# Kernel tuning notes

Measured on AMD Instinct MI355X. Metric: run time of the kernel, lower is better.

The kernel has to match this reference:

```python
import jax, jax.numpy as jnp
import numpy as np

V = 32000      # vocab_size
D = 768        # embed_dim / d_model
NL = 2         # attn_layers
BATCH = 2
T = 1024       # seq_len
ED = 2 * D     # d_inner (expand_factor=2)
NS = 16        # d_state
K = 4          # d_conv
DT_RANK = (D + 15) // 16  # ceil(d_model/16) = 48


def setup_inputs():
    key = jax.random.key(0)
    ks = jax.random.split(key, 12)
    nrm = lambda k, shp, s=0.02: (jax.random.normal(k, shp, jnp.float32) * s)
    tokens = jax.random.randint(ks[0], (BATCH, T), 0, V)
    embed = nrm(ks[1], (V, D))
    in_proj_w = nrm(ks[2], (NL, 2 * ED, D))
    conv_w = nrm(ks[3], (NL, ED, 1, K), 0.1)   # depthwise conv kernel (O=ED, I/g=1, K)
    conv_b = jnp.zeros((NL, ED), jnp.float32)
    x_proj_w = nrm(ks[4], (NL, DT_RANK + 2 * NS, ED))
    dt_proj_w = nrm(ks[5], (NL, ED, DT_RANK), 0.05)
    dt_proj_b = nrm(ks[6], (NL, ED), 0.05)
    # S4D real init: A = -[1..NS] per channel
    A_log = jnp.log(jnp.broadcast_to(jnp.arange(1, NS + 1, dtype=jnp.float32), (NL, ED, NS)))
    D_param = jnp.ones((NL, ED), jnp.float32)
    out_proj_w = nrm(ks[7], (NL, D, ED))
    ln_w = jnp.ones((NL, D), jnp.float32)
    ln_b = jnp.zeros((NL, D), jnp.float32)
    head_w = nrm(ks[8], (V, D))
    head_b = jnp.zeros((V,), jnp.float32)
    return {"tokens": tokens, "embed": embed, "in_proj_w": in_proj_w,
            "conv_w": conv_w, "conv_b": conv_b, "x_proj_w": x_proj_w,
            "dt_proj_w": dt_proj_w, "dt_proj_b": dt_proj_b, "A_log": A_log,
            "D_param": D_param, "out_proj_w": out_proj_w, "ln_w": ln_w,
            "ln_b": ln_b, "head_w": head_w, "head_b": head_b}


def silu(x):
    return x * jax.nn.sigmoid(x)


def layer_norm(x, w, b, eps=1e-5):
    mu = jnp.mean(x, axis=-1, keepdims=True)
    var = jnp.mean(jnp.square(x - mu), axis=-1, keepdims=True)
    return (x - mu) * jax.lax.rsqrt(var + eps) * w + b


def mamba_block(x, in_w, cw, cb, xp_w, dt_w, dt_b, a_log, d_par, out_w):
    # x: (B, T, D)
    xz = jnp.einsum('btd,ed->bte', x, in_w)           # (B, T, 2*ED)
    xin, z = jnp.split(xz, 2, axis=-1)                 # each (B, T, ED)
    # causal depthwise conv over time
    xc = jnp.transpose(xin, (0, 2, 1))                 # (B, ED, T)
    xc = jax.lax.conv_general_dilated(
        xc, cw, window_strides=(1,), padding=[(K - 1, 0)],
        dimension_numbers=('NCH', 'OIH', 'NCH'), feature_group_count=ED)
    xc = xc + cb[None, :, None]
    xin = silu(jnp.transpose(xc, (0, 2, 1)))           # (B, T, ED)
    # selective SSM
    A = -jnp.exp(a_log)                                # (ED, NS)
    dbc = jnp.einsum('bte,fe->btf', xin, xp_w)         # (B, T, dt_rank + 2*NS)
    delta = dbc[..., :DT_RANK]
    Bm = dbc[..., DT_RANK:DT_RANK + NS]                # (B, T, NS)
    Cm = dbc[..., DT_RANK + NS:]                       # (B, T, NS)
    delta = jax.nn.softplus(jnp.einsum('btr,er->bte', delta, dt_w) + dt_b)  # (B, T, ED)
    dA = jnp.exp(delta[..., None] * A)                 # (B, T, ED, NS)
    dBx = (delta * xin)[..., None] * Bm[:, :, None, :] # (B, T, ED, NS)

    def step(h, inp):
        dA_t, dBx_t, C_t = inp                         # (B,ED,NS),(B,ED,NS),(B,NS)
        h = dA_t * h + dBx_t
        y = jnp.einsum('ben,bn->be', h, C_t)
        return h, y

    h0 = jnp.zeros((x.shape[0], ED, NS), xin.dtype)
    _, ys = jax.lax.scan(step, h0,
                         (jnp.swapaxes(dA, 0, 1), jnp.swapaxes(dBx, 0, 1),
                          jnp.swapaxes(Cm, 0, 1)))
    y = jnp.swapaxes(ys, 0, 1) + d_par * xin           # (B, T, ED)
    return jnp.einsum('bte,de->btd', y * silu(z), out_w)


def reference(tokens, embed, in_proj_w, conv_w, conv_b, x_proj_w, dt_proj_w,
              dt_proj_b, A_log, D_param, out_proj_w, ln_w, ln_b, head_w, head_b):
    x = embed[tokens]                                  # (B, T, D)
    for l in range(NL):  # note: NO residual, matches x = ln(layer(x))
        x = layer_norm(
            mamba_block(x, in_proj_w[l], conv_w[l], conv_b[l], x_proj_w[l],
                        dt_proj_w[l], dt_proj_b[l], A_log[l], D_param[l],
                        out_proj_w[l]),
            ln_w[l], ln_b[l])
    return jnp.einsum('btd,vd->btv', x, head_w) + head_b
```

## Files before the change

### kernel.cpp

```cpp
#include <hip/hip_runtime.h>
#include <hip/hip_bf16.h>
#include <cstdint>
#include <cstddef>

using u16 = unsigned short;

#define DEV static __device__ __forceinline__

DEV float bf2f(u16 u) {
  unsigned int x = ((unsigned int)u) << 16;
  float f;
  __builtin_memcpy(&f, &x, 4);
  return f;
}

DEV u16 f2bf(float f) {
  unsigned int x;
  __builtin_memcpy(&x, &f, 4);
  unsigned int r = (x + 0x7fffu + ((x >> 16) & 1u)) >> 16;
  return (u16)r;
}

typedef __bf16 bf16x8 __attribute__((ext_vector_type(8)));
typedef float f32x4 __attribute__((ext_vector_type(4)));

DEV f32x4 mfma_bf16(bf16x8 a, bf16x8 b, f32x4 c) {
  return __builtin_amdgcn_mfma_f32_16x16x32_bf16(a, b, c, 0, 0, 0);
}

DEV void async_ld16(const void* g, void* lds) {
  __builtin_amdgcn_global_load_lds((const __attribute__((address_space(1))) void*)g,
                                   (__attribute__((address_space(3))) void*)lds,
                                   16, 0, 0);
}

__global__ __launch_bounds__(256) void k_cvt(const float* __restrict__ src,
                                             u16* __restrict__ dst, int n) {
  for (int i = blockIdx.x * 256 + threadIdx.x; i < n; i += gridDim.x * 256)
    dst[i] = f2bf(src[i]);
}

template <bool SPLIT, bool BIAS>
__global__ __launch_bounds__(256, 2) void gemm_bt(
    const u16* __restrict__ Ahi, const u16* __restrict__ Alo,
    const u16* __restrict__ Bw, float* __restrict__ Cf,
    const float* __restrict__ bias, int M, int N, int K, int ldc) {
  __shared__ __align__(16) u16 sA[128 * 64];
  __shared__ __align__(16) u16 sB[128 * 64];
  __shared__ __align__(16) u16 sAl[SPLIT ? 128 * 64 : 8];

  const int tid = threadIdx.x;
  const int wave = tid >> 6;
  const int lane = tid & 63;
  const int mBase = blockIdx.y * 128;
  const int nBase = blockIdx.x * 128;
  const int wm = wave >> 1;
  const int wn = wave & 1;

  f32x4 acc[4][4];
#pragma unroll
  for (int i = 0; i < 4; ++i)
#pragma unroll
    for (int j = 0; j < 4; ++j) acc[i][j] = f32x4{0.f, 0.f, 0.f, 0.f};

  const int rsub = lane >> 3;
  const int ksub = (lane & 7) * 8;

  for (int k0 = 0; k0 < K; k0 += 64) {
#pragma unroll
    for (int it = 0; it < 4; ++it) {
      const int chunk = it * 4 + wave;
      const int row = chunk * 8 + rsub;
      async_ld16(Ahi + (size_t)(mBase + row) * K + (k0 + ksub), (char*)sA + chunk * 1024);
      if constexpr (SPLIT)
        async_ld16(Alo + (size_t)(mBase + row) * K + (k0 + ksub), (char*)sAl + chunk * 1024);
      int rn = nBase + row;
      if (rn > N - 1) rn = N - 1;
      async_ld16(Bw + (size_t)rn * K + (k0 + ksub), (char*)sB + chunk * 1024);
    }
    __syncthreads();

    const int rr = lane & 15;
    const int q8 = (lane >> 4) * 8;
#pragma unroll
    for (int ks = 0; ks < 64; ks += 32) {
      bf16x8 aH[4], bF[4], aL[4];
#pragma unroll
      for (int i = 0; i < 4; ++i) {
        aH[i] = *(const bf16x8*)(sA + (wm * 64 + i * 16 + rr) * 64 + ks + q8);
        bF[i] = *(const bf16x8*)(sB + (wn * 64 + i * 16 + rr) * 64 + ks + q8);
        if constexpr (SPLIT)
          aL[i] = *(const bf16x8*)(sAl + (wm * 64 + i * 16 + rr) * 64 + ks + q8);
      }
#pragma unroll
      for (int i = 0; i < 4; ++i)
#pragma unroll
        for (int j = 0; j < 4; ++j) {
          acc[i][j] = mfma_bf16(aH[i], bF[j], acc[i][j]);
          if constexpr (SPLIT) acc[i][j] = mfma_bf16(aL[i], bF[j], acc[i][j]);
        }
    }
    __syncthreads();
  }

  const int r0 = (lane >> 4) * 4;
  const int cn = lane & 15;
#pragma unroll
  for (int i = 0; i < 4; ++i) {
    const int mm = mBase + wm * 64 + i * 16 + r0;
#pragma unroll
    for (int j = 0; j < 4; ++j) {
      const int nn = nBase + wn * 64 + j * 16 + cn;
      if (nn < N) {
        float bv = 0.f;
        if constexpr (BIAS) bv = bias[nn];
#pragma unroll
        for (int r = 0; r < 4; ++r)
          Cf[(size_t)(mm + r) * ldc + nn] = acc[i][j][r] + bv;
      }
    }
  }
}

__global__ __launch_bounds__(256) void k_embed(const int* __restrict__ tok,
                                               const float* __restrict__ emb,
                                               u16* __restrict__ xh,
                                               u16* __restrict__ xl) {
  const int m = blockIdx.x;
  const float* src = emb + (size_t)tok[m] * 768;
  for (int d = threadIdx.x; d < 768; d += 256) {
    const float v = src[d];
    const u16 h = f2bf(v);
    xh[(size_t)m * 768 + d] = h;
    xl[(size_t)m * 768 + d] = f2bf(v - bf2f(h));
  }
}

__global__ __launch_bounds__(256) void k_conv(const float* __restrict__ xz,
                                              const float* __restrict__ cw,
                                              const float* __restrict__ cb,
                                              float* __restrict__ xinc,
                                              u16* __restrict__ xih,
                                              u16* __restrict__ xil) {
  const int idx = blockIdx.x * 256 + threadIdx.x;
  const int e = idx % 1536;
  const int m = idx / 1536;
  const int t = m & 1023;
  const int b = m >> 10;
  float acc = cb[e];
#pragma unroll
  for (int k = 0; k < 4; ++k) {
    const int tt = t - 3 + k;
    if (tt >= 0) acc += xz[(size_t)((b << 10) + tt) * 3072 + e] * cw[e * 4 + k];
  }
  const float s = acc / (1.f + __expf(-acc));
  xinc[idx] = s;
  const u16 h = f2bf(s);
  xih[idx] = h;
  xil[idx] = f2bf(s - bf2f(h));
}

__global__ __launch_bounds__(256) void k_dt(const float* __restrict__ dbc,
                                            const float* __restrict__ dtw,
                                            const float* __restrict__ dtb,
                                            float* __restrict__ delta) {
  const int m = blockIdx.x;
  __shared__ float sd[48];
  if (threadIdx.x < 48) sd[threadIdx.x] = dbc[m * 80 + threadIdx.x];
  __syncthreads();
  for (int e = threadIdx.x; e < 1536; e += 256) {
    float acc = dtb[e];
#pragma unroll
    for (int r = 0; r < 48; ++r) acc += sd[r] * dtw[e * 48 + r];
    const float sp = (acc > 20.f) ? acc : log1pf(__expf(acc));
    delta[m * 1536 + e] = sp;
  }
}

#define SCAN_NC 16
#define SCAN_CL 64

__global__ __launch_bounds__(256) void k_scan1(
    const float* __restrict__ delta, const float* __restrict__ xinc,
    const float* __restrict__ dbc, const float* __restrict__ alog,
    float* __restrict__ chP, float* __restrict__ chQ) {
  const int b = blockIdx.y;
  const int c = blockIdx.z;
  const int e = blockIdx.x * 16 + (threadIdx.x >> 4);
  const int n = threadIdx.x & 15;
  const float Aen = -__expf(alog[e * 16 + n]);
  const int m0 = (b << 10) + c * SCAN_CL;
  float h = 0.f, P = 1.f;
  float dl = delta[m0 * 1536 + e];
  float xi = xinc[m0 * 1536 + e];
  float Bn = dbc[m0 * 80 + 48 + n];
  for (int t = 0; t < SCAN_CL; ++t) {
    const float dl_c = dl, xi_c = xi, Bn_c = Bn;
    if (t < SCAN_CL - 1) {
      const int m2 = m0 + t + 1;
      dl = delta[m2 * 1536 + e];
      xi = xinc[m2 * 1536 + e];
      Bn = dbc[m2 * 80 + 48 + n];
    }
    const float dA = __expf(dl_c * Aen);
    P *= dA;
    h = dA * h + (dl_c * xi_c) * Bn_c;
  }
  const size_t idx = (((size_t)b * SCAN_NC + c) * 1536 + e) * 16 + n;
  chP[idx] = P;
  chQ[idx] = h;
}

__global__ __launch_bounds__(256) void k_scan_fix(const float* __restrict__ chP,
                                                  const float* __restrict__ chQ,
                                                  float* __restrict__ hst) {
  const int b = blockIdx.y;
  const int e = blockIdx.x * 16 + (threadIdx.x >> 4);
  const int n = threadIdx.x & 15;
  float h = 0.f;
#pragma unroll
  for (int c = 0; c < SCAN_NC; ++c) {
    const size_t idx = (((size_t)b * SCAN_NC + c) * 1536 + e) * 16 + n;
    hst[idx] = h;
    h = chP[idx] * h + chQ[idx];
  }
}

__global__ __launch_bounds__(256) void k_scan2(
    const float* __restrict__ delta, const float* __restrict__ xinc,
    const float* __restrict__ dbc, const float* __restrict__ xz,
    const float* __restrict__ alog, const float* __restrict__ dpar,
    const float* __restrict__ hst, u16* __restrict__ ymh,
    u16* __restrict__ yml) {
  const int b = blockIdx.y;
  const int c = blockIdx.z;
  const int e = blockIdx.x * 16 + (threadIdx.x >> 4);
  const int n = threadIdx.x & 15;
  const float Aen = -__expf(alog[e * 16 + n]);
  const float dp = dpar[e];
  const int m0 = (b << 10) + c * SCAN_CL;
  float h = hst[(((size_t)b * SCAN_NC + c) * 1536 + e) * 16 + n];
  float dl = delta[m0 * 1536 + e];
  float xi = xinc[m0 * 1536 + e];
  float Bn = dbc[m0 * 80 + 48 + n];
  float Cn = dbc[m0 * 80 + 64 + n];
  float zz = xz[(size_t)m0 * 3072 + 1536 + e];
  for (int t = 0; t < SCAN_CL; ++t) {
    const float dl_c = dl, xi_c = xi, Bn_c = Bn, Cn_c = Cn, zz_c = zz;
    if (t < SCAN_CL - 1) {
      const int m2 = m0 + t + 1;
      dl = delta[m2 * 1536 + e];
      xi = xinc[m2 * 1536 + e];
      Bn = dbc[m2 * 80 + 48 + n];
      Cn = dbc[m2 * 80 + 64 + n];
      zz = xz[(size_t)m2 * 3072 + 1536 + e];
    }
    const float dA = __expf(dl_c * Aen);
    h = dA * h + (dl_c * xi_c) * Bn_c;
    float p = h * Cn_c;
    p += __shfl_xor(p, 1);
    p += __shfl_xor(p, 2);
    p += __shfl_xor(p, 4);
    p += __shfl_xor(p, 8);
    if (n == 0) {
      const float y = p + dp * xi_c;
      const float sz = zz_c / (1.f + __expf(-zz_c));
      const float ym = y * sz;
      const int mt = m0 + t;
      const u16 hh = f2bf(ym);
      ymh[mt * 1536 + e] = hh;
      yml[mt * 1536 + e] = f2bf(ym - bf2f(hh));
    }
  }
}

__global__ __launch_bounds__(256) void k_ln(const float* __restrict__ g,
                                            const float* __restrict__ w,
                                            const float* __restrict__ bb,
                                            u16* __restrict__ xh,
                                            u16* __restrict__ xl) {
  const int m = blockIdx.x;
  const float* row = g + (size_t)m * 768;
  const int tid = threadIdx.x;
  const float v0 = row[tid], v1 = row[tid + 256], v2 = row[tid + 512];
  float s = v0 + v1 + v2;
#pragma unroll
  for (int o = 32; o > 0; o >>= 1) s += __shfl_xor(s, o);
  __shared__ float red[4];
  if ((tid & 63) == 0) red[tid >> 6] = s;
  __syncthreads();
  const float mu = (red[0] + red[1] + red[2] + red[3]) * (1.f / 768.f);
  const float d0 = v0 - mu, d1 = v1 - mu, d2 = v2 - mu;
  float q = d0 * d0 + d1 * d1 + d2 * d2;
#pragma unroll
  for (int o = 32; o > 0; o >>= 1) q += __shfl_xor(q, o);
  __syncthreads();
  if ((tid & 63) == 0) red[tid >> 6] = q;
  __syncthreads();
  const float var = (red[0] + red[1] + red[2] + red[3]) * (1.f / 768.f);
  const float rs = rsqrtf(var + 1e-5f);
  const float dd[3] = {d0, d1, d2};
#pragma unroll
  for (int i = 0; i < 3; ++i) {
    const int d = tid + i * 256;
    const float y = dd[i] * rs * w[d] + bb[d];
    const u16 h = f2bf(y);
    xh[(size_t)m * 768 + d] = h;
    xl[(size_t)m * 768 + d] = f2bf(y - bf2f(h));
  }
}

extern "C" void kernel_launch(void* const* d_in, const int* in_sizes, int n_in,
                              void* d_out, int out_size, void* d_ws, size_t ws_size,
                              hipStream_t stream) {
  const int* tokens = (const int*)d_in[0];
  const float* embed = (const float*)d_in[1];
  const float* in_w = (const float*)d_in[2];
  const float* conv_w = (const float*)d_in[3];
  const float* conv_b = (const float*)d_in[4];
  const float* xp_w = (const float*)d_in[5];
  const float* dt_w = (const float*)d_in[6];
  const float* dt_b = (const float*)d_in[7];
  const float* A_log = (const float*)d_in[8];
  const float* D_par = (const float*)d_in[9];
  const float* out_w = (const float*)d_in[10];
  const float* ln_w = (const float*)d_in[11];
  const float* ln_b = (const float*)d_in[12];
  const float* head_w = (const float*)d_in[13];
  const float* head_b = (const float*)d_in[14];

  char* p = (char*)d_ws;
  auto alloc = [&](size_t bytes) {
    char* r = p;
    p += (bytes + 255) & ~(size_t)255;
    return r;
  };
  float* xz = (float*)alloc(2048ull * 3072 * 4);
  float* xinc = (float*)alloc(2048ull * 1536 * 4);
  u16* xih = (u16*)alloc(2048ull * 1536 * 2);
  u16* xil = (u16*)alloc(2048ull * 1536 * 2);
  float* dbc = (float*)alloc(2048ull * 80 * 4);
  float* delta = (float*)alloc(2048ull * 1536 * 4);
  u16* ymh = (u16*)alloc(2048ull * 1536 * 2);
  u16* yml = (u16*)alloc(2048ull * 1536 * 2);
  float* gout = (float*)alloc(2048ull * 768 * 4);
  u16* xh = (u16*)alloc(2048ull * 768 * 2);
  u16* xl = (u16*)alloc(2048ull * 768 * 2);
  u16* w_in_h = (u16*)alloc(2ull * 3072 * 768 * 2);
  u16* w_xp_h = (u16*)alloc(2ull * 80 * 1536 * 2);
  u16* w_out_h = (u16*)alloc(2ull * 768 * 1536 * 2);
  u16* w_head_h = (u16*)alloc(32000ull * 768 * 2);
  float* chP = (float*)alloc(2ull * SCAN_NC * 1536 * 16 * 4);
  float* chQ = (float*)alloc(2ull * SCAN_NC * 1536 * 16 * 4);
  float* hst = (float*)alloc(2ull * SCAN_NC * 1536 * 16 * 4);

  k_cvt<<<2048, 256, 0, stream>>>(in_w, w_in_h, 2 * 3072 * 768);
  k_cvt<<<256, 256, 0, stream>>>(xp_w, w_xp_h, 2 * 80 * 1536);
  k_cvt<<<1024, 256, 0, stream>>>(out_w, w_out_h, 2 * 768 * 1536);
  k_cvt<<<4096, 256, 0, stream>>>(head_w, w_head_h, 32000 * 768);

  k_embed<<<2048, 256, 0, stream>>>(tokens, embed, xh, xl);

  for (int l = 0; l < 2; ++l) {
    gemm_bt<true, false><<<dim3(24, 16), 256, 0, stream>>>(
        xh, xl, w_in_h + (size_t)l * 2359296, xz, nullptr, 2048, 3072, 768, 3072);

    k_conv<<<12288, 256, 0, stream>>>(xz, conv_w + l * 6144, conv_b + l * 1536, xinc, xih, xil);

    gemm_bt<true, false><<<dim3(1, 16), 256, 0, stream>>>(
        xih, xil, w_xp_h + (size_t)l * 122880, dbc, nullptr, 2048, 80, 1536, 80);

    k_dt<<<2048, 256, 0, stream>>>(dbc, dt_w + (size_t)l * 73728, dt_b + l * 1536, delta);

    k_scan1<<<dim3(96, 2, SCAN_NC), 256, 0, stream>>>(
        delta, xinc, dbc, A_log + l * 24576, chP, chQ);
    k_scan_fix<<<dim3(96, 2), 256, 0, stream>>>(chP, chQ, hst);
    k_scan2<<<dim3(96, 2, SCAN_NC), 256, 0, stream>>>(
        delta, xinc, dbc, xz, A_log + l * 24576, D_par + l * 1536, hst, ymh, yml);

    gemm_bt<true, false><<<dim3(6, 16), 256, 0, stream>>>(
        ymh, yml, w_out_h + (size_t)l * 1179648, gout, nullptr, 2048, 768, 1536, 768);

    k_ln<<<2048, 256, 0, stream>>>(gout, ln_w + l * 768, ln_b + l * 768, xh, xl);
  }

  gemm_bt<true, true><<<dim3(250, 16), 256, 0, stream>>>(
      xh, xl, w_head_h, (float*)d_out, head_b, 2048, 32000, 768, 32000);
}
```

Before: 1.316 ms.

## Add double-buffered 128x256 swizzled GEMM and split-K atomics for skinny GEMMs

Adds a new 512-thread GEMM kernel with 128x256 tiles, double-buffered async LDS staging, XOR-swizzled LDS layout, workgroup remapping and MFMA priority hints. It is used for the in_proj and head projections. The x_proj and out_proj GEMMs switch to split-K with atomicAdd into zero-initialised outputs to expose more parallelism. The cost is extra zeroing kernels and atomic traffic, and float atomics make the accumulation order non-deterministic.

```diff
diff --git a/kernel.cpp b/kernel.cpp
--- a/kernel.cpp
+++ b/kernel.cpp
@@ -40,11 +40,130 @@
     dst[i] = f2bf(src[i]);
 }
 
+__global__ __launch_bounds__(256) void k_zero(float* __restrict__ p, int n) {
+  const int i = blockIdx.x * 256 + threadIdx.x;
+  if (i < n) p[i] = 0.f;
+}
+
 template <bool SPLIT, bool BIAS>
+__global__ __launch_bounds__(512, 2) void gemm2(
+    const u16* __restrict__ Ahi, const u16* __restrict__ Alo,
+    const u16* __restrict__ Bw, float* __restrict__ Cf,
+    const float* __restrict__ bias, int M, int N, int K, int ldc) {
+  __shared__ __align__(16) u16 sA[2][128 * 64];
+  __shared__ __align__(16) u16 sAl[SPLIT ? 2 : 1][128 * 64];
+  __shared__ __align__(16) u16 sB[2][256 * 64];
+
+  const int tid = threadIdx.x;
+  const int wave = tid >> 6;
+  const int lane = tid & 63;
+  const int nwg = gridDim.x;
+  const int w = (blockIdx.x & 7) * (nwg >> 3) + (blockIdx.x >> 3);
+  const int mBlocks = M >> 7;
+  const int mb = w % mBlocks;
+  const int nb = w / mBlocks;
+  const int mBase = mb * 128;
+  const int nBase = nb * 256;
+  const int wm = wave >> 2;
+  const int wn = wave & 3;
+
+  f32x4 acc[4][4];
+#pragma unroll
+  for (int i = 0; i < 4; ++i)
+#pragma unroll
+    for (int j = 0; j < 4; ++j) acc[i][j] = f32x4{0.f, 0.f, 0.f, 0.f};
+
+  const int rl = lane >> 3;
+  const int sw = (lane & 7) ^ rl;
+
+  auto stage = [&](int bf, int k0) {
+    const int koff = k0 + sw * 8;
+#pragma unroll
+    for (int r = 0; r < 2; ++r) {
+      const int row = r * 64 + wave * 8;
+      async_ld16(Ahi + (size_t)(mBase + row + rl) * K + koff,
+                 (u16*)sA[bf] + row * 64);
+    }
+    if constexpr (SPLIT) {
+#pragma unroll
+      for (int r = 0; r < 2; ++r) {
+        const int row = r * 64 + wave * 8;
+        async_ld16(Alo + (size_t)(mBase + row + rl) * K + koff,
+                   (u16*)sAl[bf] + row * 64);
+      }
+    }
+#pragma unroll
+    for (int r = 0; r < 4; ++r) {
+      const int row = r * 64 + wave * 8;
+      async_ld16(Bw + (size_t)(nBase + row + rl) * K + koff,
+                 (u16*)sB[bf] + row * 64);
+    }
+  };
+
+  const int rr = lane & 15;
+  const int qh = lane >> 4;
+
+  stage(0, 0);
+  __syncthreads();
+
+  const int nt = K >> 6;
+  int cur = 0;
+  for (int t = 0; t < nt; ++t) {
+    if (t + 1 < nt) stage(cur ^ 1, (t + 1) * 64);
+#pragma unroll
+    for (int ph = 0; ph < 4; ++ph) {
+      const int ks = (ph >> 1) * 32;
+      const int ih = (ph & 1) * 2;
+      const int q = (ks >> 3) + qh;
+      bf16x8 aH[2], aL[2], bF[4];
+#pragma unroll
+      for (int i = 0; i < 2; ++i) {
+        const int ra = wm * 64 + (ih + i) * 16 + rr;
+        const int off = ra * 64 + ((q ^ (ra & 7)) << 3);
+        aH[i] = *(const bf16x8*)((const u16*)sA[cur] + off);
+        if constexpr (SPLIT) aL[i] = *(const bf16x8*)((const u16*)sAl[cur] + off);
+      }
+#pragma unroll
+      for (int j = 0; j < 4; ++j) {
+        const int rb = wn * 64 + j * 16 + rr;
+        bF[j] = *(const bf16x8*)((const u16*)sB[cur] + rb * 64 + ((q ^ (rb & 7)) << 3));
+      }
+      __builtin_amdgcn_s_setprio(1);
+#pragma unroll
+      for (int i = 0; i < 2; ++i)
+#pragma unroll
+        for (int j = 0; j < 4; ++j) {
+          acc[ih + i][j] = mfma_bf16(aH[i], bF[j], acc[ih + i][j]);
+          if constexpr (SPLIT) acc[ih + i][j] = mfma_bf16(aL[i], bF[j], acc[ih + i][j]);
+        }
+      __builtin_amdgcn_s_setprio(0);
+    }
+    __syncthreads();
+    cur ^= 1;
+  }
+
+  const int r0 = (lane >> 4) * 4;
+  const int cn = lane & 15;
+#pragma unroll
+  for (int i = 0; i < 4; ++i) {
+    const int mm = mBase + wm * 64 + i * 16 + r0;
+#pragma unroll
+    for (int j = 0; j < 4; ++j) {
+      const int nn = nBase + wn * 64 + j * 16 + cn;
+      float bv = 0.f;
+      if constexpr (BIAS) bv = bias[nn];
+#pragma unroll
+      for (int r = 0; r < 4; ++r)
+        Cf[(size_t)(mm + r) * ldc + nn] = acc[i][j][r] + bv;
+    }
+  }
+}
+
+template <bool SPLIT, bool BIAS, bool ATOMIC>
 __global__ __launch_bounds__(256, 2) void gemm_bt(
     const u16* __restrict__ Ahi, const u16* __restrict__ Alo,
     const u16* __restrict__ Bw, float* __restrict__ Cf,
-    const float* __restrict__ bias, int M, int N, int K, int ldc) {
+    const float* __restrict__ bias, int M, int N, int K, int ldc, int kChunk) {
   __shared__ __align__(16) u16 sA[128 * 64];
   __shared__ __align__(16) u16 sB[128 * 64];
   __shared__ __align__(16) u16 sAl[SPLIT ? 128 * 64 : 8];
@@ -54,6 +173,7 @@
   const int lane = tid & 63;
   const int mBase = blockIdx.y * 128;
   const int nBase = blockIdx.x * 128;
+  const int kBeg = blockIdx.z * kChunk;
   const int wm = wave >> 1;
   const int wn = wave & 1;
 
@@ -66,7 +186,7 @@
   const int rsub = lane >> 3;
   const int ksub = (lane & 7) * 8;
 
-  for (int k0 = 0; k0 < K; k0 += 64) {
+  for (int k0 = kBeg; k0 < kBeg + kChunk; k0 += 64) {
 #pragma unroll
     for (int it = 0; it < 4; ++it) {
       const int chunk = it * 4 + wave;
@@ -115,8 +235,12 @@
         float bv = 0.f;
         if constexpr (BIAS) bv = bias[nn];
 #pragma unroll
-        for (int r = 0; r < 4; ++r)
-          Cf[(size_t)(mm + r) * ldc + nn] = acc[i][j][r] + bv;
+        for (int r = 0; r < 4; ++r) {
+          if constexpr (ATOMIC)
+            atomicAdd(&Cf[(size_t)(mm + r) * ldc + nn], acc[i][j][r]);
+          else
+            Cf[(size_t)(mm + r) * ldc + nn] = acc[i][j][r] + bv;
+        }
       }
     }
   }
@@ -362,13 +486,14 @@
   k_embed<<<2048, 256, 0, stream>>>(tokens, embed, xh, xl);
 
   for (int l = 0; l < 2; ++l) {
-    gemm_bt<true, false><<<dim3(24, 16), 256, 0, stream>>>(
+    gemm2<true, false><<<12 * 16, 512, 0, stream>>>(
         xh, xl, w_in_h + (size_t)l * 2359296, xz, nullptr, 2048, 3072, 768, 3072);
 
     k_conv<<<12288, 256, 0, stream>>>(xz, conv_w + l * 6144, conv_b + l * 1536, xinc, xih, xil);
 
-    gemm_bt<true, false><<<dim3(1, 16), 256, 0, stream>>>(
-        xih, xil, w_xp_h + (size_t)l * 122880, dbc, nullptr, 2048, 80, 1536, 80);
+    k_zero<<<640, 256, 0, stream>>>(dbc, 2048 * 80);
+    gemm_bt<true, false, true><<<dim3(1, 16, 12), 256, 0, stream>>>(
+        xih, xil, w_xp_h + (size_t)l * 122880, dbc, nullptr, 2048, 80, 1536, 80, 128);
 
     k_dt<<<2048, 256, 0, stream>>>(dbc, dt_w + (size_t)l * 73728, dt_b + l * 1536, delta);
 
@@ -378,12 +503,13 @@
     k_scan2<<<dim3(96, 2, SCAN_NC), 256, 0, stream>>>(
         delta, xinc, dbc, xz, A_log + l * 24576, D_par + l * 1536, hst, ymh, yml);
 
-    gemm_bt<true, false><<<dim3(6, 16), 256, 0, stream>>>(
-        ymh, yml, w_out_h + (size_t)l * 1179648, gout, nullptr, 2048, 768, 1536, 768);
+    k_zero<<<6144, 256, 0, stream>>>(gout, 2048 * 768);
+    gemm_bt<true, false, true><<<dim3(6, 16, 8), 256, 0, stream>>>(
+        ymh, yml, w_out_h + (size_t)l * 1179648, gout, nullptr, 2048, 768, 1536, 768, 192);
 
     k_ln<<<2048, 256, 0, stream>>>(gout, ln_w + l * 768, ln_b + l * 768, xh, xl);
   }
 
-  gemm_bt<true, true><<<dim3(250, 16), 256, 0, stream>>>(
+  gemm2<true, true><<<125 * 16, 512, 0, stream>>>(
       xh, xl, w_head_h, (float*)d_out, head_b, 2048, 32000, 768, 32000);
 }
```

Result: faster. 1.289 ms (-2.1%).
